# Optimization experiments

Measured on AMD Instinct MI355X. Metric: run time of the kernel, lower is better.

Reference implementation:

```python
import jax, jax.numpy as jnp
import numpy as np

N_NODES = 50000
N_REL = 500
N_EDGES = 600000
F_OUT = 128
N_HEAD = 4


def setup_inputs() -> dict:
    key = jax.random.key(0)
    k1, k2, k3, k4, k5, k6, k7 = jax.random.split(key, 7)
    h = jax.random.normal(k1, (N_NODES, F_OUT), dtype=jnp.float32)
    inputr = jax.random.normal(k2, (N_REL, F_OUT), dtype=jnp.float32)
    # diag per-head scaling params (n_head-1, 1, f_out), near 1 so cumulative products stay sane
    w = 1.0 + 0.1 * jax.random.normal(k3, (N_HEAD - 1, 1, F_OUT), dtype=jnp.float32)
    # attention params, std = 1/sqrt(2*f_out) as in the torch init
    stdv = 1.0 / np.sqrt(2 * F_OUT)
    a_src_dst = stdv * jax.random.normal(k4, (N_HEAD, 2, F_OUT, 1), dtype=jnp.float32)
    # edge list A: [dst, rel, src]; ensure every node has at least one in-edge so the
    # softmax rowsum normalization never divides by zero
    dst_extra = jax.random.randint(k5, (N_EDGES - N_NODES,), 0, N_NODES)
    dst = jnp.concatenate([jnp.arange(N_NODES), dst_extra]).astype(jnp.int64)
    rel = jax.random.randint(k6, (N_EDGES,), 0, N_REL).astype(jnp.int64)
    src = jax.random.randint(k7, (N_EDGES,), 0, N_NODES).astype(jnp.int64)
    A = jnp.stack([dst, rel, src])  # [3, E]
    return {"h": h, "inputr": inputr, "w": w, "a_src_dst": a_src_dst, "A": A}


def reference(h, inputr, w, a_src_dst, A):
    n_head = a_src_dst.shape[0]
    N = h.shape[0]
    dst, rel, src = A[0], A[1], A[2]
    rel_feat = inputr[rel]  # [E, f_out] gathered relation features (fixed across heads)
    outputs = []
    for i in range(n_head):
        if i >= 1:
            h = h * w[i - 1]  # cumulative diagonal scaling, matches torch in-place update
        h_src = h[src]  # [E, f_out]
        # edge attention logit: h_src @ a_src + rel @ a_dst  -> [E]
        edge_logit = (h_src @ a_src_dst[i, 0] + rel_feat @ a_src_dst[i, 1])[:, 0]
        edge_e = jnp.exp(-jax.nn.leaky_relu(edge_logit, negative_slope=0.2))  # [E]
        e_rowsum = jax.ops.segment_sum(edge_e, dst, num_segments=N)  # [N]
        msg = (h_src - rel_feat) * edge_e[:, None]  # [E, f_out]
        h_prime = jax.ops.segment_sum(msg, dst, num_segments=N)  # [N, f_out]
        outputs.append(h_prime / e_rowsum[:, None])
    return jnp.stack(outputs)  # [n_head, N, f_out]
```

## Files before the change

kernel.cpp:

```cpp
#include <hip/hip_runtime.h>
#include <math.h>

#define F_OUT 128
#define N_HEAD 4
#define SCAN_CHUNK 2048

#define WS_SRCDOT  0
#define WS_RELDOT  800000
#define WS_COUNTS  808000
#define WS_OFFSETS 1008000
#define WS_CURSOR  1208016
#define WS_BSUM    1408016
#define WS_SPK     1408528

__global__ __launch_bounds__(256)
void fused_pre(const float* __restrict__ h, const float* __restrict__ inputr,
               const float* __restrict__ w, const float* __restrict__ a,
               const int* __restrict__ A,
               float* __restrict__ srcdot, float* __restrict__ reldot,
               int* __restrict__ counts,
               int N, int NREL, int E, int SB, int RB) {
    int blk = blockIdx.x;
    int t = threadIdx.x;
    int lane = t & 63;

    if (blk < SB) {
        int n = blk * 4 + (t >> 6);
        if (n >= N) return;
        float c1a = w[lane],            c1b = w[64 + lane];
        float c2a = c1a * w[F_OUT + lane], c2b = c1b * w[F_OUT + 64 + lane];
        float c3a = c2a * w[2 * F_OUT + lane], c3b = c2b * w[2 * F_OUT + 64 + lane];
        float cwa[N_HEAD] = {1.0f, c1a, c2a, c3a};
        float cwb[N_HEAD] = {1.0f, c1b, c2b, c3b};
        float x0 = h[n * F_OUT + lane];
        float x1 = h[n * F_OUT + 64 + lane];
        float p[N_HEAD];
        #pragma unroll
        for (int i = 0; i < N_HEAD; ++i)
            p[i] = x0 * (cwa[i] * a[(i * 2) * F_OUT + lane])
                 + x1 * (cwb[i] * a[(i * 2) * F_OUT + 64 + lane]);
        #pragma unroll
        for (int off = 32; off > 0; off >>= 1) {
            #pragma unroll
            for (int i = 0; i < N_HEAD; ++i) p[i] += __shfl_down(p[i], off);
        }
        if (lane == 0)
            *(float4*)(srcdot + n * 4) = make_float4(p[0], p[1], p[2], p[3]);
    } else if (blk < SB + RB) {
        int r = (blk - SB) * 4 + (t >> 6);
        if (r >= NREL) return;
        float x0 = inputr[r * F_OUT + lane];
        float x1 = inputr[r * F_OUT + 64 + lane];
        float p[N_HEAD];
        #pragma unroll
        for (int i = 0; i < N_HEAD; ++i)
            p[i] = x0 * a[(i * 2 + 1) * F_OUT + lane]
                 + x1 * a[(i * 2 + 1) * F_OUT + 64 + lane];
        #pragma unroll
        for (int off = 32; off > 0; off >>= 1) {
            #pragma unroll
            for (int i = 0; i < N_HEAD; ++i) p[i] += __shfl_down(p[i], off);
        }
        if (lane == 0)
            *(float4*)(reldot + r * 4) = make_float4(p[0], p[1], p[2], p[3]);
    } else {
        int hb = blk - SB - RB;
        #pragma unroll
        for (int k = 0; k < 4; ++k) {
            int e = (hb * 4 + k) * 256 + t;
            if (e < E) atomicAdd(&counts[A[e]], 1);
        }
    }
}

__global__ __launch_bounds__(256)
void block_sum_kernel(const int* __restrict__ counts, int* __restrict__ bsum, int N) {
    int blk = blockIdx.x, t = threadIdx.x;
    int base = blk * SCAN_CHUNK;
    int s = 0;
    #pragma unroll
    for (int k = 0; k < 8; ++k) {
        int idx = base + t + k * 256;
        if (idx < N) s += counts[idx];
    }
    #pragma unroll
    for (int off = 32; off > 0; off >>= 1) s += __shfl_down(s, off);
    __shared__ int red[4];
    if ((t & 63) == 0) red[t >> 6] = s;
    __syncthreads();
    if (t == 0) bsum[blk] = red[0] + red[1] + red[2] + red[3];
}

__global__ __launch_bounds__(256)
void scan_write_kernel(const int* __restrict__ counts, const int* __restrict__ bsum,
                       int* __restrict__ offsets, int* __restrict__ cursor,
                       int N, int NB, int E) {
    __shared__ int tsum[256];
    __shared__ int bbase_sh;
    int blk = blockIdx.x, t = threadIdx.x;
    if (t < 64) {
        int own = (t < NB) ? bsum[t] : 0;
        int v = own;
        #pragma unroll
        for (int off = 1; off < 64; off <<= 1) {
            int u = __shfl_up(v, off);
            if (t >= off) v += u;
        }
        if (t == blk) bbase_sh = v - own;
    }
    int base = blk * SCAN_CHUNK + t * 8;
    int v[8];
    #pragma unroll
    for (int k = 0; k < 8; ++k) {
        int idx = base + k;
        v[k] = (idx < N) ? counts[idx] : 0;
    }
    int s = 0;
    #pragma unroll
    for (int k = 0; k < 8; ++k) { int t0 = v[k]; v[k] = s; s += t0; }
    tsum[t] = s;
    __syncthreads();
    for (int off = 1; off < 256; off <<= 1) {
        int u = (t >= off) ? tsum[t - off] : 0;
        __syncthreads();
        tsum[t] += u;
        __syncthreads();
    }
    int tbase = bbase_sh + ((t == 0) ? 0 : tsum[t - 1]);
    #pragma unroll
    for (int k = 0; k < 8; ++k) {
        int idx = base + k;
        if (idx < N) {
            int o = tbase + v[k];
            offsets[idx] = o;
            cursor[idx] = o;
        }
    }
    if (blk == 0 && t == 0) offsets[N] = E;
}

__global__ __launch_bounds__(256)
void scatter_kernel(const int* __restrict__ A, int* __restrict__ cursor,
                    unsigned* __restrict__ sPK, int E) {
    #pragma unroll
    for (int k = 0; k < 4; ++k) {
        int e = (blockIdx.x * 4 + k) * 256 + threadIdx.x;
        if (e < E) {
            int dst = A[e];
            int rel = A[E + e];
            int src = A[2 * E + e];
            int idx = atomicAdd(&cursor[dst], 1);
            sPK[idx] = ((unsigned)rel << 16) | (unsigned)src;
        }
    }
}

#define STAGE 128
__global__ void __launch_bounds__(128)
node_kernel(const float* __restrict__ h, const float* __restrict__ inputr,
            const float* __restrict__ w,
            const float* __restrict__ srcdot, const float* __restrict__ reldot,
            const int* __restrict__ offsets, const unsigned* __restrict__ sPK,
            float* __restrict__ out, int N) {
    __shared__ float4 see[STAGE];
    __shared__ unsigned spk[STAGE];
    int n = blockIdx.x;
    int c = threadIdx.x;
    int s0 = offsets[n];
    int s1 = offsets[n + 1];
    float a1[N_HEAD] = {0, 0, 0, 0};
    float a2[N_HEAD] = {0, 0, 0, 0};
    float rs[N_HEAD] = {0, 0, 0, 0};
    for (int base = s0; base < s1; base += STAGE) {
        int cnt = min(STAGE, s1 - base);
        if (c < cnt) {
            unsigned pk = sPK[base + c];
            spk[c] = pk;
            float4 sd = *(const float4*)(srcdot + (pk & 0xFFFFu) * 4);
            float4 rd = *(const float4*)(reldot + (pk >> 16) * 4);
            float4 ee;
            float l;
            l = sd.x + rd.x; ee.x = __expf(-(l > 0.0f ? l : 0.2f * l));
            l = sd.y + rd.y; ee.y = __expf(-(l > 0.0f ? l : 0.2f * l));
            l = sd.z + rd.z; ee.z = __expf(-(l > 0.0f ? l : 0.2f * l));
            l = sd.w + rd.w; ee.w = __expf(-(l > 0.0f ? l : 0.2f * l));
            see[c] = ee;
        }
        __syncthreads();
        #pragma unroll 4
        for (int j = 0; j < cnt; ++j) {
            float4 ee = see[j];
            unsigned pk = spk[j];
            float hc = h[(pk & 0xFFFFu) * F_OUT + c];
            float rc = inputr[(pk >> 16) * F_OUT + c];
            a1[0] += hc * ee.x;  a2[0] += rc * ee.x;  rs[0] += ee.x;
            a1[1] += hc * ee.y;  a2[1] += rc * ee.y;  rs[1] += ee.y;
            a1[2] += hc * ee.z;  a2[2] += rc * ee.z;  rs[2] += ee.z;
            a1[3] += hc * ee.w;  a2[3] += rc * ee.w;  rs[3] += ee.w;
        }
        __syncthreads();
    }
    float cw1 = w[c];
    float cw2 = cw1 * w[F_OUT + c];
    float cw3 = cw2 * w[2 * F_OUT + c];
    float cwv[N_HEAD] = {1.0f, cw1, cw2, cw3};
    #pragma unroll
    for (int i = 0; i < N_HEAD; ++i) {
        out[((size_t)i * N + n) * F_OUT + c] = (cwv[i] * a1[i] - a2[i]) / rs[i];
    }
}

extern "C" void kernel_launch(void* const* d_in, const int* in_sizes, int n_in,
                              void* d_out, int out_size, void* d_ws, size_t ws_size,
                              hipStream_t stream) {
    const float* h      = (const float*)d_in[0];
    const float* inputr = (const float*)d_in[1];
    const float* w      = (const float*)d_in[2];
    const float* a      = (const float*)d_in[3];
    const int*   A      = (const int*)d_in[4];
    float* out = (float*)d_out;

    int N    = in_sizes[0] / F_OUT;
    int NREL = in_sizes[1] / F_OUT;
    int E    = in_sizes[4] / 3;
    int NB   = (N + SCAN_CHUNK - 1) / SCAN_CHUNK;
    int SB   = (N + 3) / 4;
    int RB   = (NREL + 3) / 4;
    int HB   = (E + 1023) / 1024;

    char* ws = (char*)d_ws;
    float*    srcdot  = (float*)(ws + WS_SRCDOT);
    float*    reldot  = (float*)(ws + WS_RELDOT);
    int*      counts  = (int*)(ws + WS_COUNTS);
    int*      offsets = (int*)(ws + WS_OFFSETS);
    int*      cursor  = (int*)(ws + WS_CURSOR);
    int*      bsum    = (int*)(ws + WS_BSUM);
    unsigned* sPK     = (unsigned*)(ws + WS_SPK);

    hipMemsetAsync(counts, 0, (size_t)N * sizeof(int), stream);

    fused_pre<<<SB + RB + HB, 256, 0, stream>>>(h, inputr, w, a, A, srcdot, reldot,
                                                counts, N, NREL, E, SB, RB);
    block_sum_kernel<<<NB, 256, 0, stream>>>(counts, bsum, N);
    scan_write_kernel<<<NB, 256, 0, stream>>>(counts, bsum, offsets, cursor, N, NB, E);
    scatter_kernel<<<(E + 1023) / 1024, 256, 0, stream>>>(A, cursor, sPK, E);
    node_kernel<<<N, 128, 0, stream>>>(h, inputr, w, srcdot, reldot,
                                       offsets, sPK, out, N);
}
```

Baseline: 250.2 us.

## Process two nodes per block with one wavefront per node and float2 loads

The node aggregation kernel now gives each 128-thread block two destination nodes, one 64-lane wavefront per node, and each lane handles two feature columns through float2 loads and stores. The edge attention weights for both nodes' edge ranges are staged together in shared memory, and each wavefront walks only its own subrange. This halves the block count and widens the memory accesses, cutting per-block launch and sync overhead for nodes with few in-edges. The cost is more registers per thread, and the two wavefronts in a block can be unevenly loaded when their degrees differ.

```diff
diff --git a/kernel.cpp b/kernel.cpp
--- a/kernel.cpp
+++ b/kernel.cpp
@@ -164,18 +164,32 @@
             float* __restrict__ out, int N) {
     __shared__ float4 see[STAGE];
     __shared__ unsigned spk[STAGE];
-    int n = blockIdx.x;
-    int c = threadIdx.x;
-    int s0 = offsets[n];
-    int s1 = offsets[n + 1];
-    float a1[N_HEAD] = {0, 0, 0, 0};
-    float a2[N_HEAD] = {0, 0, 0, 0};
-    float rs[N_HEAD] = {0, 0, 0, 0};
-    for (int base = s0; base < s1; base += STAGE) {
-        int cnt = min(STAGE, s1 - base);
-        if (c < cnt) {
-            unsigned pk = sPK[base + c];
-            spk[c] = pk;
+    int t = threadIdx.x;
+    int lane = t & 63;
+    int n0 = blockIdx.x * 2;
+    int n = n0 + (t >> 6);
+    int ntop = min(n0 + 2, N);
+
+    int S0 = offsets[n0];
+    int S2 = offsets[ntop];
+    int s_lo, s_hi;
+    if (n < N) { s_lo = offsets[n]; s_hi = offsets[n + 1]; }
+    else       { s_lo = S2; s_hi = S2; }
+
+    float2 a1[N_HEAD], a2[N_HEAD];
+    float rs[N_HEAD];
+    #pragma unroll
+    for (int i = 0; i < N_HEAD; ++i) {
+        a1[i] = make_float2(0.f, 0.f);
+        a2[i] = make_float2(0.f, 0.f);
+        rs[i] = 0.f;
+    }
+
+    for (int base = S0; base < S2; base += STAGE) {
+        int cnt = min(STAGE, S2 - base);
+        if (t < cnt) {
+            unsigned pk = sPK[base + t];
+            spk[t] = pk;
             float4 sd = *(const float4*)(srcdot + (pk & 0xFFFFu) * 4);
             float4 rd = *(const float4*)(reldot + (pk >> 16) * 4);
             float4 ee;
@@ -184,29 +198,48 @@
             l = sd.y + rd.y; ee.y = __expf(-(l > 0.0f ? l : 0.2f * l));
             l = sd.z + rd.z; ee.z = __expf(-(l > 0.0f ? l : 0.2f * l));
             l = sd.w + rd.w; ee.w = __expf(-(l > 0.0f ? l : 0.2f * l));
-            see[c] = ee;
-        }
-        __syncthreads();
+            see[t] = ee;
+        }
+        __syncthreads();
+        int j0 = max(s_lo, base) - base;
+        int j1 = min(s_hi, base + cnt) - base;
         #pragma unroll 4
-        for (int j = 0; j < cnt; ++j) {
+        for (int j = j0; j < j1; ++j) {
             float4 ee = see[j];
             unsigned pk = spk[j];
-            float hc = h[(pk & 0xFFFFu) * F_OUT + c];
-            float rc = inputr[(pk >> 16) * F_OUT + c];
-            a1[0] += hc * ee.x;  a2[0] += rc * ee.x;  rs[0] += ee.x;
-            a1[1] += hc * ee.y;  a2[1] += rc * ee.y;  rs[1] += ee.y;
-            a1[2] += hc * ee.z;  a2[2] += rc * ee.z;  rs[2] += ee.z;
-            a1[3] += hc * ee.w;  a2[3] += rc * ee.w;  rs[3] += ee.w;
-        }
-        __syncthreads();
-    }
-    float cw1 = w[c];
-    float cw2 = cw1 * w[F_OUT + c];
-    float cw3 = cw2 * w[2 * F_OUT + c];
-    float cwv[N_HEAD] = {1.0f, cw1, cw2, cw3};
-    #pragma unroll
-    for (int i = 0; i < N_HEAD; ++i) {
-        out[((size_t)i * N + n) * F_OUT + c] = (cwv[i] * a1[i] - a2[i]) / rs[i];
+            float2 hc = *(const float2*)(h + (pk & 0xFFFFu) * F_OUT + lane * 2);
+            float2 rc = *(const float2*)(inputr + (pk >> 16) * F_OUT + lane * 2);
+            a1[0].x += hc.x * ee.x; a1[0].y += hc.y * ee.x;
+            a2[0].x += rc.x * ee.x; a2[0].y += rc.y * ee.x;
+            rs[0] += ee.x;
+            a1[1].x += hc.x * ee.y; a1[1].y += hc.y * ee.y;
+            a2[1].x += rc.x * ee.y; a2[1].y += rc.y * ee.y;
+            rs[1] += ee.y;
+            a1[2].x += hc.x * ee.z; a1[2].y += hc.y * ee.z;
+            a2[2].x += rc.x * ee.z; a2[2].y += rc.y * ee.z;
+            rs[2] += ee.z;
+            a1[3].x += hc.x * ee.w; a1[3].y += hc.y * ee.w;
+            a2[3].x += rc.x * ee.w; a2[3].y += rc.y * ee.w;
+            rs[3] += ee.w;
+        }
+        __syncthreads();
+    }
+
+    if (n < N) {
+        float2 w0 = *(const float2*)(w + lane * 2);
+        float2 w1 = *(const float2*)(w + F_OUT + lane * 2);
+        float2 w2 = *(const float2*)(w + 2 * F_OUT + lane * 2);
+        float2 cw1 = w0;
+        float2 cw2 = make_float2(cw1.x * w1.x, cw1.y * w1.y);
+        float2 cw3 = make_float2(cw2.x * w2.x, cw2.y * w2.y);
+        float2 cwv[N_HEAD] = {make_float2(1.f, 1.f), cw1, cw2, cw3};
+        #pragma unroll
+        for (int i = 0; i < N_HEAD; ++i) {
+            float2 o;
+            o.x = (cwv[i].x * a1[i].x - a2[i].x) / rs[i];
+            o.y = (cwv[i].y * a1[i].y - a2[i].y) / rs[i];
+            *(float2*)(out + ((size_t)i * N + n) * F_OUT + lane * 2) = o;
+        }
     }
 }
 
@@ -244,6 +277,6 @@
     block_sum_kernel<<<NB, 256, 0, stream>>>(counts, bsum, N);
     scan_write_kernel<<<NB, 256, 0, stream>>>(counts, bsum, offsets, cursor, N, NB, E);
     scatter_kernel<<<(E + 1023) / 1024, 256, 0, stream>>>(A, cursor, sPK, E);
-    node_kernel<<<N, 128, 0, stream>>>(h, inputr, w, srcdot, reldot,
-                                       offsets, sPK, out, N);
-}
+    node_kernel<<<(N + 1) / 2, 128, 0, stream>>>(h, inputr, w, srcdot, reldot,
+                                                 offsets, sPK, out, N);
+}
```

Result: no change. 252.5 us (+0.9%).
